# Performance work log

Measured on AMD Instinct MI355X. Metric: run time of the kernel, lower is better.

Reference implementation:

```python
import jax, jax.numpy as jnp
import numpy as np

N = 20000      # nodes
E = 320000     # edges (avg degree 16)
C = 128        # channels (num_features from hidden_irreps 128x0e+128x1o)
R = 8          # radial basis size
S = 10         # num_species
H = 64         # radial MLP hidden
M = 16         # MLP_irreps = 16x0e
AVG_NEIGH = 16.0


def setup_inputs() -> dict:
    key = jax.random.key(0)
    ks = jax.random.split(key, 24)
    d = {}
    d["vectors"] = jax.random.normal(ks[0], (E, 3), jnp.float32)
    d["lengths"] = jax.random.uniform(ks[1], (E, 1), jnp.float32)
    d["node_feats"] = jax.random.normal(ks[2], (N, C), jnp.float32)
    species = jax.random.randint(ks[3], (N,), 0, S)
    d["node_attrs"] = jax.nn.one_hot(species, S, dtype=jnp.float32)
    d["edge_feats"] = jax.random.normal(ks[4], (E, R), jnp.float32)
    d["edge_index"] = jax.random.randint(ks[5], (2, E), 0, N)
    p = lambda k, shape, sc: jax.random.normal(k, shape, jnp.float32) * sc
    d["W_up"] = p(ks[6], (C, C), C ** -0.5)
    d["radial_w1"] = p(ks[7], (R + 1, H), (R + 1) ** -0.5)
    d["radial_b1"] = jnp.zeros((H,), jnp.float32)
    d["radial_w2"] = p(ks[8], (H, 2 * C), H ** -0.5)
    d["Wd0"] = p(ks[9], (C, C), C ** -0.5)
    d["Wd1"] = p(ks[10], (C, C), C ** -0.5)
    d["Wprod0"] = p(ks[11], (S, 5, C), 1.0)   # per-species symmetric-contraction weights, 0e paths
    d["Wprod1"] = p(ks[12], (S, 4, C), 1.0)   # per-species weights, 1o paths
    d["Wp0"] = p(ks[13], (C, C), C ** -0.5)
    d["Wp1"] = p(ks[14], (C, C), C ** -0.5)
    d["Wr1"] = p(ks[15], (C, M), C ** -0.5)
    d["Wr2"] = p(ks[16], (M, C), M ** -0.5)
    d["Wg"] = p(ks[17], (M, 1), M ** -0.5)
    d["wv"] = p(ks[18], (C, 1), C ** -0.5)
    return d


def _forward(vectors, lengths, node_feats, node_attrs, edge_feats,
             W_up, radial_w1, radial_b1, radial_w2, Wd0, Wd1,
             Wprod0, Wprod1, Wp0, Wp1, Wr1, Wr2, Wg, wv, edge_index):
    senders, receivers = edge_index[0], edge_index[1]
    # --- spherical harmonics (normalize=True), l=0 constant, l=1 ~ sqrt(3)*unit_vec ---
    u = vectors / (jnp.linalg.norm(vectors, axis=1, keepdims=True) + 1e-9)
    Y1 = jnp.sqrt(3.0) * u                                    # [E,3]
    # --- DiffusionInteractionBlock: linear up, radial-weighted tp conv, scatter, linear down ---
    h = node_feats @ W_up                                     # [N,C]
    hs = h[senders]                                           # [E,C] gather
    rad_in = jnp.concatenate([edge_feats, lengths], axis=1)   # [E,R+1]
    rad = jax.nn.silu(rad_in @ radial_w1 + radial_b1) @ radial_w2  # [E,2C]
    w0, w1 = rad[:, :C], rad[:, C:]
    m0 = w0 * hs                                              # [E,C]   0e x 0e -> 0e
    m1 = (w1 * hs)[:, None, :] * Y1[:, :, None]               # [E,3,C] 0e x 1o -> 1o
    s0 = jax.ops.segment_sum(m0, receivers, num_segments=N) / AVG_NEIGH
    s1 = jax.ops.segment_sum(m1, receivers, num_segments=N) / AVG_NEIGH
    a0 = s0 @ Wd0                                             # [N,C]
    a1 = s1 @ Wd1                                             # [N,3,C]
    # --- EquivariantProductBasisBlock: symmetric contraction, correlation=3, per-species weights ---
    dot11 = jnp.sum(a1 * a1, axis=1)                          # [N,C]  1o.1o -> 0e
    paths0 = jnp.stack([a0, a0 * a0, dot11, a0 ** 3, a0 * dot11], axis=1)          # [N,5,C]
    paths1 = jnp.stack([a1, a0[:, None, :] * a1, (a0 ** 2)[:, None, :] * a1,
                        dot11[:, None, :] * a1], axis=1)                            # [N,4,3,C]
    b0 = jnp.einsum('ns,spc,npc->nc', node_attrs, Wprod0, paths0)
    b1 = jnp.einsum('ns,spc,npic->nic', node_attrs, Wprod1, paths1)
    h0 = b0 @ Wp0                                             # [N,C]
    h1 = b1 @ Wp1                                             # [N,3,C]
    # --- NonLinearReadoutBlock: gated MLP readout ---
    mh = jax.nn.silu(h0 @ Wr1)                                # [N,M]
    scalars = mh @ Wr2                                        # [N,C]
    gate = jax.nn.silu(mh @ Wg)                               # [N,1]
    vec = (h1 @ wv)[..., 0] * gate                            # [N,3]
    nf = jnp.concatenate([h0, h1.reshape(N, 3 * C)], axis=1)  # [N,4C]
    return scalars, vec, nf


def reference(vectors, lengths, node_feats, node_attrs, edge_feats, edge_index,
              W_up, radial_w1, radial_b1, radial_w2, Wd0, Wd1,
              Wprod0, Wprod1, Wp0, Wp1, Wr1, Wr2, Wg, wv):
    # returns (node_out[:, :-3], node_out[:, -3:], node_feats)
    return _forward(vectors, lengths, node_feats, node_attrs, edge_feats,
                    W_up, radial_w1, radial_b1, radial_w2, Wd0, Wd1,
                    Wprod0, Wprod1, Wp0, Wp1, Wr1, Wr2, Wg, wv, edge_index)
```

## Files before the change

### kernel.cpp

```cpp
#include <hip/hip_runtime.h>

#define NN 20000
#define NE 320000
#define CC 128
#define SS 10
#define NWIN 10000

typedef __attribute__((ext_vector_type(8))) short short8;
typedef __attribute__((ext_vector_type(4))) float f32x4;

#define MFMA16(a, b, c) __builtin_amdgcn_mfma_f32_16x16x32_bf16(a, b, c, 0, 0, 0)

__device__ __forceinline__ float silu_f(float x) { return x / (1.f + __expf(-x)); }

__device__ __forceinline__ unsigned short f2bf(float x) {
  unsigned u = __float_as_uint(x);
  unsigned r = u + 0x7FFFu + ((u >> 16) & 1u);
  return (unsigned short)(r >> 16);
}
__device__ __forceinline__ float bf2f(unsigned short h) {
  return __uint_as_float(((unsigned)h) << 16);
}
__device__ __forceinline__ void cvt8(const float* xs, short8& ah, short8& al) {
#pragma unroll
  for (int j = 0; j < 8; ++j) {
    const unsigned short h = f2bf(xs[j]);
    ah[j] = (short)h;
    al[j] = (short)f2bf(xs[j] - bf2f(h));
  }
}

__global__ __launch_bounds__(256) void k_prep_w2(const float* __restrict__ W2,
                                                 unsigned short* __restrict__ w2h,
                                                 unsigned short* __restrict__ w2l) {
  const int i = blockIdx.x * 256 + threadIdx.x;
  if (i < 64 * 256) {
    const int col = i % 256, k = i / 256;
    const float x = W2[i];
    const unsigned short h = f2bf(x);
    w2h[col * 64 + k] = h;
    w2l[col * 64 + k] = f2bf(x - bf2f(h));
  }
}

__global__ __launch_bounds__(256) void k_prep_w128(
    const float* __restrict__ Wd0, const float* __restrict__ Wd1,
    const float* __restrict__ Wp0, const float* __restrict__ Wp1,
    unsigned short* __restrict__ wh, unsigned short* __restrict__ wl) {
  const int b = blockIdx.x;
  const int m = b >> 6;
  const int i = (b & 63) * 256 + threadIdx.x;
  const float* W = (m == 0) ? Wd0 : (m == 1) ? Wd1 : (m == 2) ? Wp0 : Wp1;
  const int k = i >> 7, col = i & 127;
  const float x = W[i];
  const unsigned short h = f2bf(x);
  wh[m * 16384 + col * 128 + k] = h;
  wl[m * 16384 + col * 128 + k] = f2bf(x - bf2f(h));
}

__global__ __launch_bounds__(128) void k_node_h(const float* __restrict__ nf,
                                                const float* __restrict__ W,
                                                float* __restrict__ h) {
  __shared__ __align__(16) float rows[8][CC];
  const int c = threadIdx.x;
  const int n0 = blockIdx.x * 8;
#pragma unroll
  for (int q = 0; q < 8; ++q) rows[q][c] = nf[(n0 + q) * CC + c];
  __syncthreads();
  float acc[8] = {0.f, 0.f, 0.f, 0.f, 0.f, 0.f, 0.f, 0.f};
  for (int k = 0; k < CC; k += 4) {
    const float w0 = W[(k + 0) * CC + c];
    const float w1 = W[(k + 1) * CC + c];
    const float w2 = W[(k + 2) * CC + c];
    const float w3 = W[(k + 3) * CC + c];
#pragma unroll
    for (int q = 0; q < 8; ++q) {
      float4 v = *(const float4*)&rows[q][k];
      acc[q] += v.x * w0 + v.y * w1 + v.z * w2 + v.w * w3;
    }
  }
#pragma unroll
  for (int q = 0; q < 8; ++q) h[(n0 + q) * CC + c] = acc[q];
}

__global__ void k_hist(const int* __restrict__ recv, int* __restrict__ cnt) {
  int i = blockIdx.x * blockDim.x + threadIdx.x;
  if (i < NE) atomicAdd(&cnt[recv[i]], 1);
}

__global__ __launch_bounds__(1024) void k_scan2(int* cntcur, int* offs) {
  const int t = threadIdx.x;
  int v[20];
  int tot = 0;
  if (t < 1000) {
#pragma unroll
    for (int i = 0; i < 20; ++i) {
      v[i] = cntcur[t * 20 + i];
      tot += v[i];
    }
  }
  const int lane = t & 63;
  int x = tot;
#pragma unroll
  for (int off = 1; off < 64; off <<= 1) {
    int y = __shfl_up(x, off, 64);
    if (lane >= off) x += y;
  }
  __shared__ int wt[16], wo[16];
  if (lane == 63) wt[t >> 6] = x;
  __syncthreads();
  if (t == 0) {
    int a = 0;
    for (int w = 0; w < 16; ++w) {
      wo[w] = a;
      a += wt[w];
    }
    offs[NN] = a;
  }
  __syncthreads();
  int run = wo[t >> 6] + x - tot;
  if (t < 1000) {
#pragma unroll
    for (int i = 0; i < 20; ++i) {
      offs[t * 20 + i] = run;
      cntcur[t * 20 + i] = run;
      run += v[i];
    }
  }
}

__global__ void k_fill2(const int* __restrict__ recv, const int* __restrict__ snd,
                        const float* __restrict__ vectors,
                        const float* __restrict__ lengths,
                        const float* __restrict__ efeat, int* __restrict__ cur,
                        float* __restrict__ edata) {
  int i = blockIdx.x * blockDim.x + threadIdx.x;
  if (i < NE) {
    const int r = recv[i];
    const int pos = atomicAdd(&cur[r], 1);
    const float vx = vectors[i * 3 + 0];
    const float vy = vectors[i * 3 + 1];
    const float vz = vectors[i * 3 + 2];
    const float nr = sqrtf(vx * vx + vy * vy + vz * vz) + 1e-9f;
    const float sc = 1.7320508075688772f / nr;
    float4 a = {vx * sc, vy * sc, vz * sc, lengths[i]};
    float4 b = *(const float4*)&efeat[(size_t)i * 8];
    float4 c = *(const float4*)&efeat[(size_t)i * 8 + 4];
    float4 d;
    ((int*)&d)[0] = snd[i];
    d.y = 0.f; d.z = 0.f; d.w = 0.f;
    float* rec = edata + (size_t)pos * 16;
    *(float4*)rec = a;
    *(float4*)(rec + 4) = b;
    *(float4*)(rec + 8) = c;
    *(float4*)(rec + 12) = d;
  }
}

__global__ __launch_bounds__(256) void k_edge3p(
    const float* __restrict__ hbuf, const float* __restrict__ W1,
    const float* __restrict__ B1, const unsigned short* __restrict__ w2h,
    const unsigned short* __restrict__ w2l, const int* __restrict__ offs,
    const float* __restrict__ edata, float* __restrict__ sout) {
  __shared__ __align__(16) float W1s[9 * 64];
  __shared__ __align__(16) float B1s[64];
  __shared__ __align__(16) float ed[2][32][20];
  __shared__ __align__(16) unsigned short hidh[32][72];
  __shared__ __align__(16) unsigned short hidl[32][72];

  const int t = threadIdx.x;
  const int l = t & 63, wv = t >> 6, lg = l >> 4, lm = l & 15;
  const int half = wv & 1;
  const bool isw1 = wv >= 2;

  for (int i = t; i < 576; i += 256) W1s[i] = W1[i];
  if (t < 64) B1s[t] = B1[t];

  short8 Bh[4][2], Bl[4][2];
#pragma unroll
  for (int ct = 0; ct < 4; ++ct)
#pragma unroll
    for (int s = 0; s < 2; ++s) {
      const int col = wv * 64 + ct * 16 + lm;
      Bh[ct][s] = *(const short8*)&w2h[col * 64 + s * 32 + lg * 8];
      Bl[ct][s] = *(const short8*)&w2l[col * 64 + s * 32 + lg * 8];
    }

  const int se = t >> 1, sq = t & 1;
  const int se2 = t >> 2, sq2 = t & 3;

#define CONSUME(GR, ACC, HC, YA, YB, YC)                                       \
  do {                                                                         \
    float vvv[4][4];                                                           \
    _Pragma("unroll") for (int ct = 0; ct < 4; ++ct)                           \
        _Pragma("unroll") for (int r = 0; r < 4; ++r)                          \
            vvv[ct][r] = (ACC)[ct][r] * (HC)[ct][r];                           \
    const bool fast0 = ((GR) + 16 <= o1);                                      \
    const bool fast1 = ((GR) >= o1) && ((GR) + 16 <= o2);                      \
    if (fast0) {                                                               \
      if (!isw1) {                                                             \
        _Pragma("unroll") for (int ct = 0; ct < 4; ++ct)                       \
            _Pragma("unroll") for (int r = 0; r < 4; ++r)                      \
                p0[0][ct] += vvv[ct][r];                                       \
      } else {                                                                 \
        _Pragma("unroll") for (int ct = 0; ct < 4; ++ct)                       \
            _Pragma("unroll") for (int r = 0; r < 4; ++r) {                    \
          px[0][ct] += vvv[ct][r] * (YA)[r];                                   \
          py[0][ct] += vvv[ct][r] * (YB)[r];                                   \
          pz[0][ct] += vvv[ct][r] * (YC)[r];                                   \
        }                                                                      \
      }                                                                        \
    } else if (fast1) {                                                        \
      if (!isw1) {                                                             \
        _Pragma("unroll") for (int ct = 0; ct < 4; ++ct)                       \
            _Pragma("unroll") for (int r = 0; r < 4; ++r)                      \
                p0[1][ct] += vvv[ct][r];                                       \
      } else {                                                                 \
        _Pragma("unroll") for (int ct = 0; ct < 4; ++ct)                       \
            _Pragma("unroll") for (int r = 0; r < 4; ++r) {                    \
          px[1][ct] += vvv[ct][r] * (YA)[r];                                   \
          py[1][ct] += vvv[ct][r] * (YB)[r];                                   \
          pz[1][ct] += vvv[ct][r] * (YC)[r];                                   \
        }                                                                      \
      }                                                                        \
    } else {                                                                   \
      const int grow0 = (GR) + lg * 4;                                         \
      _Pragma("unroll") for (int sl = 0; sl < 2; ++sl) {                       \
        const int slo = sl ? o1 : o0;                                          \
        const int shi = sl ? o2 : o1;                                          \
        if (shi > (GR) && slo < (GR) + 16) {                                   \
          if (!isw1) {                                                         \
            _Pragma("unroll") for (int r = 0; r < 4; ++r) {                    \
              const bool in = (grow0 + r >= slo) && (grow0 + r < shi);         \
              _Pragma("unroll") for (int ct = 0; ct < 4; ++ct)                 \
                  p0[sl][ct] += in ? vvv[ct][r] : 0.f;                         \
            }                                                                  \
          } else {                                                             \
            _Pragma("unroll") for (int r = 0; r < 4; ++r) {                    \
              const bool in = (grow0 + r >= slo) && (grow0 + r < shi);         \
              _Pragma("unroll") for (int ct = 0; ct < 4; ++ct) {               \
                const float m = in ? vvv[ct][r] : 0.f;                         \
                px[sl][ct] += m * (YA)[r];                                     \
                py[sl][ct] += m * (YB)[r];                                     \
                pz[sl][ct] += m * (YC)[r];                                     \
              }                                                                \
            }                                                                  \
          }                                                                    \
        }                                                                      \
      }                                                                        \
    }                                                                          \
  } while (0)

  __syncthreads();

  for (int win = blockIdx.x; win < NWIN; win += gridDim.x) {
    const int nb = win * 2;
    const int o0 = offs[nb], o1 = offs[nb + 1], o2 = offs[nb + 2];

    float p0[2][4] = {};
    float px[2][4] = {}, py[2][4] = {}, pz[2][4] = {};

    float4 sreg = {0.f, 0.f, 0.f, 0.f};
    if (t < 128) {
      const int idx = o0 + se2;
      if (idx < o2) sreg = *(const float4*)&edata[(size_t)idx * 16 + sq2 * 4];
      *(float4*)&ed[0][se2][sq2 * 4] = sreg;
      sreg = (float4){0.f, 0.f, 0.f, 0.f};
      const int idx1 = o0 + 32 + se2;
      if (idx1 < o2) sreg = *(const float4*)&edata[(size_t)idx1 * 16 + sq2 * 4];
    }
    __syncthreads();

    const int npass = (o2 - o0 + 31) >> 5;
    for (int p = 0; p < npass; ++p) {
      const int pb = p & 1;
      const int base = o0 + p * 32;
      {
        const int e = t & 31, kseg = t >> 5;
        const int k0 = kseg * 8;
        float ef[9];
#pragma unroll
        for (int r = 0; r < 8; ++r) ef[r] = ed[pb][e][4 + r];
        ef[8] = ed[pb][e][3];
        float4 xa = *(const float4*)&B1s[k0];
        float4 xb = *(const float4*)&B1s[k0 + 4];
#pragma unroll
        for (int r = 0; r < 9; ++r) {
          const float4 wa = *(const float4*)&W1s[r * 64 + k0];
          const float4 wb = *(const float4*)&W1s[r * 64 + k0 + 4];
          xa.x += ef[r] * wa.x; xa.y += ef[r] * wa.y;
          xa.z += ef[r] * wa.z; xa.w += ef[r] * wa.w;
          xb.x += ef[r] * wb.x; xb.y += ef[r] * wb.y;
          xb.z += ef[r] * wb.z; xb.w += ef[r] * wb.w;
        }
        float xs[8];
        xs[0] = silu_f(xa.x); xs[1] = silu_f(xa.y);
        xs[2] = silu_f(xa.z); xs[3] = silu_f(xa.w);
        xs[4] = silu_f(xb.x); xs[5] = silu_f(xb.y);
        xs[6] = silu_f(xb.z); xs[7] = silu_f(xb.w);
        short8 ah, al;
        cvt8(xs, ah, al);
        *(short8*)&hidh[e][k0] = ah;
        *(short8*)&hidl[e][k0] = al;
      }
      __syncthreads();
      if (t < 128) {
        *(float4*)&ed[pb ^ 1][se2][sq2 * 4] = sreg;
        sreg = (float4){0.f, 0.f, 0.f, 0.f};
        const int idx2 = base + 64 + se2;
        if (idx2 < o2) sreg = *(const float4*)&edata[(size_t)idx2 * 16 + sq2 * 4];
      }
      {
        int sd0[4];
        float ya0[4], yb0[4], yc0[4];
#pragma unroll
        for (int r = 0; r < 4; ++r) {
          const int row = lg * 4 + r;
          sd0[r] = __float_as_int(ed[pb][row][12]);
          ya0[r] = ed[pb][row][0];
          yb0[r] = ed[pb][row][1];
          yc0[r] = ed[pb][row][2];
        }
        float hc0[4][4];
#pragma unroll
        for (int ct = 0; ct < 4; ++ct) {
          const int col = half * 64 + ct * 16 + lm;
#pragma unroll
          for (int r = 0; r < 4; ++r) hc0[ct][r] = hbuf[(size_t)sd0[r] * CC + col];
        }
        short8 Ah0 = *(const short8*)&hidh[lm][lg * 8];
        short8 Ah1 = *(const short8*)&hidh[lm][32 + lg * 8];
        short8 Al0 = *(const short8*)&hidl[lm][lg * 8];
        short8 Al1 = *(const short8*)&hidl[lm][32 + lg * 8];
        f32x4 acc0[4];
#pragma unroll
        for (int ct = 0; ct < 4; ++ct) {
          f32x4 a = {0.f, 0.f, 0.f, 0.f};
          a = MFMA16(Ah0, Bh[ct][0], a);
          a = MFMA16(Ah0, Bl[ct][0], a);
          a = MFMA16(Al0, Bh[ct][0], a);
          a = MFMA16(Ah1, Bh[ct][1], a);
          a = MFMA16(Ah1, Bl[ct][1], a);
          a = MFMA16(Al1, Bh[ct][1], a);
          acc0[ct] = a;
        }
        const bool live1 = (base + 16) < o2;
        if (live1) {
          int sd1[4];
          float ya1[4], yb1[4], yc1[4];
#pragma unroll
          for (int r = 0; r < 4; ++r) {
            const int row = 16 + lg * 4 + r;
            sd1[r] = __float_as_int(ed[pb][row][12]);
            ya1[r] = ed[pb][row][0];
            yb1[r] = ed[pb][row][1];
            yc1[r] = ed[pb][row][2];
          }
          float hc1[4][4];
#pragma unroll
          for (int ct = 0; ct < 4; ++ct) {
            const int col = half * 64 + ct * 16 + lm;
#pragma unroll
            for (int r = 0; r < 4; ++r) hc1[ct][r] = hbuf[(size_t)sd1[r] * CC + col];
          }
          CONSUME(base, acc0, hc0, ya0, yb0, yc0);
          short8 Bh0_ = *(const short8*)&hidh[16 + lm][lg * 8];
          short8 Bh1_ = *(const short8*)&hidh[16 + lm][32 + lg * 8];
          short8 Bl0_ = *(const short8*)&hidl[16 + lm][lg * 8];
          short8 Bl1_ = *(const short8*)&hidl[16 + lm][32 + lg * 8];
          f32x4 acc1[4];
#pragma unroll
          for (int ct = 0; ct < 4; ++ct) {
            f32x4 a = {0.f, 0.f, 0.f, 0.f};
            a = MFMA16(Bh0_, Bh[ct][0], a);
            a = MFMA16(Bh0_, Bl[ct][0], a);
            a = MFMA16(Bl0_, Bh[ct][0], a);
            a = MFMA16(Bh1_, Bh[ct][1], a);
            a = MFMA16(Bh1_, Bl[ct][1], a);
            a = MFMA16(Bl1_, Bh[ct][1], a);
            acc1[ct] = a;
          }
          CONSUME(base + 16, acc1, hc1, ya1, yb1, yc1);
        } else {
          CONSUME(base, acc0, hc0, ya0, yb0, yc0);
        }
      }
      __syncthreads();
    }

    const float inv = 1.f / 16.f;
#pragma unroll
    for (int sl = 0; sl < 2; ++sl) {
      const int n = nb + sl;
      if (!isw1) {
#pragma unroll
        for (int ct = 0; ct < 4; ++ct) {
          float v = p0[sl][ct];
          v += __shfl_xor(v, 16, 64);
          v += __shfl_xor(v, 32, 64);
          if (lg == 0) sout[(size_t)n * 512 + half * 64 + ct * 16 + lm] = v * inv;
        }
      } else {
#pragma unroll
        for (int ct = 0; ct < 4; ++ct) {
          float vx = px[sl][ct], vy = py[sl][ct], vz = pz[sl][ct];
          vx += __shfl_xor(vx, 16, 64); vx += __shfl_xor(vx, 32, 64);
          vy += __shfl_xor(vy, 16, 64); vy += __shfl_xor(vy, 32, 64);
          vz += __shfl_xor(vz, 16, 64); vz += __shfl_xor(vz, 32, 64);
          if (lg == 0) {
            const int c = half * 64 + ct * 16 + lm;
            sout[(size_t)n * 512 + 128 + c] = vx * inv;
            sout[(size_t)n * 512 + 256 + c] = vy * inv;
            sout[(size_t)n * 512 + 384 + c] = vz * inv;
          }
        }
      }
    }
  }
#undef CONSUME
}

__global__ __launch_bounds__(256, 2) void k_down3(
    const float* __restrict__ sbuf, const float* __restrict__ attrs,
    const unsigned short* __restrict__ wbh, const unsigned short* __restrict__ wbl,
    const float* __restrict__ Wprod0, const float* __restrict__ Wprod1,
    const float* __restrict__ Wr1, const float* __restrict__ Wr2,
    const float* __restrict__ Wg, const float* __restrict__ wvv,
    float* __restrict__ out_scalars, float* __restrict__ out_vec,
    float* __restrict__ out_nf) {
  __shared__ __align__(16) char smem[35840];
  __shared__ int sidx_s[16];
  __shared__ float mh_s[16][17];
  __shared__ float gate_s[16];
  unsigned short* bh = (unsigned short*)smem;
  unsigned short* bl = bh + 8960;
  float* hX = (float*)smem;

  const int t = threadIdx.x;
  const int l = t & 63, wv = t >> 6, lg = l >> 4, lm = l & 15;
  const int n0 = blockIdx.x * 16;

  if (t < 16) {
    int si = 0;
#pragma unroll
    for (int s = 0; s < SS; ++s)
      si = (attrs[(size_t)(n0 + t) * SS + s] > 0.5f) ? s : si;
    sidx_s[t] = si;
  }

  short8 Wfh[2][2][4], Wfl[2][2][4];
#pragma unroll
  for (int mat = 0; mat < 2; ++mat)
#pragma unroll
    for (int ct = 0; ct < 2; ++ct)
#pragma unroll
      for (int ks = 0; ks < 4; ++ks) {
        const size_t off =
            (size_t)mat * 16384 + (size_t)(wv * 32 + ct * 16 + lm) * 128 + ks * 32 + lg * 8;
        Wfh[mat][ct][ks] = *(const short8*)&wbh[off];
        Wfl[mat][ct][ks] = *(const short8*)&wbl[off];
      }

  f32x4 acc[4][2];
#pragma unroll 1
  for (int comp = 0; comp < 4; ++comp) {
    short8 Ah[4], Al[4];
#pragma unroll
    for (int ks = 0; ks < 4; ++ks) {
      const size_t so = (size_t)(n0 + lm) * 512 + comp * 128 + ks * 32 + lg * 8;
      const float4 xa = *(const float4*)&sbuf[so];
      const float4 xb = *(const float4*)&sbuf[so + 4];
      float xs[8] = {xa.x, xa.y, xa.z, xa.w, xb.x, xb.y, xb.z, xb.w};
      cvt8(xs, Ah[ks], Al[ks]);
    }
    const int mat = comp ? 1 : 0;
#pragma unroll
    for (int ct = 0; ct < 2; ++ct) {
      f32x4 a = {0.f, 0.f, 0.f, 0.f};
#pragma unroll
      for (int ks = 0; ks < 4; ++ks) {
        a = MFMA16(Ah[ks], Wfh[mat][ct][ks], a);
        a = MFMA16(Ah[ks], Wfl[mat][ct][ks], a);
        a = MFMA16(Al[ks], Wfh[mat][ct][ks], a);
      }
      acc[comp][ct] = a;
    }
  }

#pragma unroll
  for (int ct = 0; ct < 2; ++ct) {
#pragma unroll
    for (int r = 0; r < 4; ++r) {
      const int node = lg * 4 + r;
      const int c = wv * 32 + ct * 16 + lm;
      const int si = sidx_s[node];
      const float a0 = acc[0][ct][r];
      const float ax = acc[1][ct][r], ay = acc[2][ct][r], az = acc[3][ct][r];
      const float dot = ax * ax + ay * ay + az * az;
      const float a2 = a0 * a0;
      const float* w0 = Wprod0 + (size_t)si * 5 * CC;
      const float* w1 = Wprod1 + (size_t)si * 4 * CC;
      const float b0v = w0[c] * a0 + w0[CC + c] * a2 + w0[2 * CC + c] * dot +
                        w0[3 * CC + c] * (a2 * a0) + w0[4 * CC + c] * (a0 * dot);
      const float fac =
          w1[c] + w1[CC + c] * a0 + w1[2 * CC + c] * a2 + w1[3 * CC + c] * dot;
      const float bv[4] = {b0v, ax * fac, ay * fac, az * fac};
#pragma unroll
      for (int m = 0; m < 4; ++m) {
        const int idx = (m * 16 + node) * 140 + c;
        const unsigned short h = f2bf(bv[m]);
        bh[idx] = h;
        bl[idx] = f2bf(bv[m] - bf2f(h));
      }
    }
  }

#pragma unroll
  for (int mat = 0; mat < 2; ++mat)
#pragma unroll
    for (int ct = 0; ct < 2; ++ct)
#pragma unroll
      for (int ks = 0; ks < 4; ++ks) {
        const size_t off = (size_t)(2 + mat) * 16384 +
                           (size_t)(wv * 32 + ct * 16 + lm) * 128 + ks * 32 + lg * 8;
        Wfh[mat][ct][ks] = *(const short8*)&wbh[off];
        Wfl[mat][ct][ks] = *(const short8*)&wbl[off];
      }
  __syncthreads();

  f32x4 acch[4][2];
#pragma unroll 1
  for (int comp = 0; comp < 4; ++comp) {
    short8 Ah[4], Al[4];
#pragma unroll
    for (int ks = 0; ks < 4; ++ks) {
      const int idx = (comp * 16 + lm) * 140 + ks * 32 + lg * 8;
      Ah[ks] = *(const short8*)&bh[idx];
      Al[ks] = *(const short8*)&bl[idx];
    }
    const int mat = comp ? 1 : 0;
#pragma unroll
    for (int ct = 0; ct < 2; ++ct) {
      f32x4 a = {0.f, 0.f, 0.f, 0.f};
#pragma unroll
      for (int ks = 0; ks < 4; ++ks) {
        a = MFMA16(Ah[ks], Wfh[mat][ct][ks], a);
        a = MFMA16(Ah[ks], Wfl[mat][ct][ks], a);
        a = MFMA16(Al[ks], Wfh[mat][ct][ks], a);
      }
      acch[comp][ct] = a;
    }
  }
  __syncthreads();

#pragma unroll
  for (int comp = 0; comp < 4; ++comp)
#pragma unroll
    for (int ct = 0; ct < 2; ++ct)
#pragma unroll
      for (int r = 0; r < 4; ++r) {
        const int node = lg * 4 + r;
        const int c = wv * 32 + ct * 16 + lm;
        hX[(comp * 16 + node) * 132 + c] = acch[comp][ct][r];
        out_nf[(size_t)(n0 + node) * 512 + comp * 128 + c] = acch[comp][ct][r];
      }
  __syncthreads();

  {
    const int node = t >> 4, m = t & 15;
    float a = 0.f;
    const float* Xn = &hX[node * 132];
    for (int k = 0; k < CC; k += 4) {
      const float4 h4 = *(const float4*)&Xn[k];
      a += h4.x * Wr1[(k + 0) * 16 + m] + h4.y * Wr1[(k + 1) * 16 + m] +
           h4.z * Wr1[(k + 2) * 16 + m] + h4.w * Wr1[(k + 3) * 16 + m];
    }
    mh_s[node][m] = silu_f(a);
  }
  __syncthreads();
  if (t < 16) {
    float g = 0.f;
#pragma unroll
    for (int m = 0; m < 16; ++m) g += mh_s[t][m] * Wg[m];
    gate_s[t] = silu_f(g);
  }
  __syncthreads();
  {
    const int node = t >> 4, cb = (t & 15) * 8;
#pragma unroll
    for (int j = 0; j < 8; ++j) {
      float a = 0.f;
#pragma unroll
      for (int m = 0; m < 16; ++m) a += mh_s[node][m] * Wr2[m * CC + cb + j];
      out_scalars[(size_t)(n0 + node) * CC + cb + j] = a;
    }
  }
  if (t < 48) {
    const int node = t / 3, i = t % 3;
    float a = 0.f;
    const float* Xn = &hX[((1 + i) * 16 + node) * 132];
    for (int k = 0; k < CC; k += 4) {
      const float4 h4 = *(const float4*)&Xn[k];
      const float4 w4 = *(const float4*)&wvv[k];
      a += h4.x * w4.x + h4.y * w4.y + h4.z * w4.z + h4.w * w4.w;
    }
    out_vec[(size_t)(n0 + node) * 3 + i] = a * gate_s[node];
  }
}

extern "C" void kernel_launch(void* const* d_in, const int* in_sizes, int n_in,
                              void* d_out, int out_size, void* d_ws, size_t ws_size,
                              hipStream_t stream) {
  const float* vectors    = (const float*)d_in[0];
  const float* lengths    = (const float*)d_in[1];
  const float* node_feats = (const float*)d_in[2];
  const float* node_attrs = (const float*)d_in[3];
  const float* edge_feats = (const float*)d_in[4];
  const int*   edge_index = (const int*)d_in[5];
  const float* W_up       = (const float*)d_in[6];
  const float* radial_w1  = (const float*)d_in[7];
  const float* radial_b1  = (const float*)d_in[8];
  const float* radial_w2  = (const float*)d_in[9];
  const float* Wd0        = (const float*)d_in[10];
  const float* Wd1        = (const float*)d_in[11];
  const float* Wprod0     = (const float*)d_in[12];
  const float* Wprod1     = (const float*)d_in[13];
  const float* Wp0        = (const float*)d_in[14];
  const float* Wp1        = (const float*)d_in[15];
  const float* Wr1        = (const float*)d_in[16];
  const float* Wr2        = (const float*)d_in[17];
  const float* Wg         = (const float*)d_in[18];
  const float* wv         = (const float*)d_in[19];

  float* out = (float*)d_out;
  float* out_scalars = out;
  float* out_vec = out + (size_t)NN * CC;
  float* out_nf = out + (size_t)NN * CC + (size_t)NN * 3;
  float* sbuf = out_nf;
  float* hbuf = out_scalars;

  int* cnt = (int*)d_ws;
  int* offs = cnt + NN;
  float* edata = (float*)(offs + NN + 4);
  unsigned short* w2h = (unsigned short*)(edata + (size_t)NE * 16);
  unsigned short* w2l = w2h + 16384;
  unsigned short* wbh = w2l + 16384;
  unsigned short* wbl = wbh + 4 * 16384;

  const int* senders = edge_index;
  const int* receivers = edge_index + NE;

  hipMemsetAsync(cnt, 0, NN * sizeof(int), stream);
  k_prep_w2<<<64, 256, 0, stream>>>(radial_w2, w2h, w2l);
  k_prep_w128<<<256, 256, 0, stream>>>(Wd0, Wd1, Wp0, Wp1, wbh, wbl);
  k_node_h<<<NN / 8, 128, 0, stream>>>(node_feats, W_up, hbuf);
  k_hist<<<NE / 256, 256, 0, stream>>>(receivers, cnt);
  k_scan2<<<1, 1024, 0, stream>>>(cnt, offs);
  k_fill2<<<NE / 256, 256, 0, stream>>>(receivers, senders, vectors, lengths,
                                        edge_feats, cnt, edata);
  k_edge3p<<<2048, 256, 0, stream>>>(hbuf, radial_w1, radial_b1, w2h, w2l,
                                     offs, edata, sbuf);
  k_down3<<<NN / 16, 256, 0, stream>>>(sbuf, node_attrs, wbh, wbl, Wprod0,
                                       Wprod1, Wr1, Wr2, Wg, wv,
                                       out_scalars, out_vec, out_nf);
}
```

Before: 311.2 us.

## Split edge kernel columns so each wave handles both radial halves for 32 channels

Changes the per-wave work split in the edge convolution kernel. Previously two waves handled the scalar-path radial weights and two handled the vector-path weights, each across 64 channels. Now every wave computes both radial halves for its own 32 channels. The sender feature gather (hbuf) per wave drops from 64 to 32 columns, and the edge product is reused for both the scalar and vector accumulations. The MFMA count per wave and the register footprint stay about the same, and all waves now follow the same uniform code path.

```diff
diff --git a/kernel.cpp b/kernel.cpp
--- a/kernel.cpp
+++ b/kernel.cpp
@@ -157,7 +157,7 @@
   }
 }
 
-__global__ __launch_bounds__(256) void k_edge3p(
+__global__ __launch_bounds__(256) void k_edge3q(
     const float* __restrict__ hbuf, const float* __restrict__ W1,
     const float* __restrict__ B1, const unsigned short* __restrict__ w2h,
     const unsigned short* __restrict__ w2l, const int* __restrict__ offs,
@@ -170,58 +170,50 @@
 
   const int t = threadIdx.x;
   const int l = t & 63, wv = t >> 6, lg = l >> 4, lm = l & 15;
-  const int half = wv & 1;
-  const bool isw1 = wv >= 2;
 
   for (int i = t; i < 576; i += 256) W1s[i] = W1[i];
   if (t < 64) B1s[t] = B1[t];
 
-  short8 Bh[4][2], Bl[4][2];
-#pragma unroll
-  for (int ct = 0; ct < 4; ++ct)
+  short8 B0h[2][2], B0l[2][2], B1h[2][2], B1l[2][2];
+#pragma unroll
+  for (int ct = 0; ct < 2; ++ct)
 #pragma unroll
     for (int s = 0; s < 2; ++s) {
-      const int col = wv * 64 + ct * 16 + lm;
-      Bh[ct][s] = *(const short8*)&w2h[col * 64 + s * 32 + lg * 8];
-      Bl[ct][s] = *(const short8*)&w2l[col * 64 + s * 32 + lg * 8];
-    }
-
-  const int se = t >> 1, sq = t & 1;
+      const int col0 = wv * 32 + ct * 16 + lm;
+      const int col1 = 128 + col0;
+      B0h[ct][s] = *(const short8*)&w2h[col0 * 64 + s * 32 + lg * 8];
+      B0l[ct][s] = *(const short8*)&w2l[col0 * 64 + s * 32 + lg * 8];
+      B1h[ct][s] = *(const short8*)&w2h[col1 * 64 + s * 32 + lg * 8];
+      B1l[ct][s] = *(const short8*)&w2l[col1 * 64 + s * 32 + lg * 8];
+    }
+
   const int se2 = t >> 2, sq2 = t & 3;
 
-#define CONSUME(GR, ACC, HC, YA, YB, YC)                                       \
+#define CONSUME(GR, A0, A1, HC, YA, YB, YC)                                    \
   do {                                                                         \
-    float vvv[4][4];                                                           \
-    _Pragma("unroll") for (int ct = 0; ct < 4; ++ct)                           \
-        _Pragma("unroll") for (int r = 0; r < 4; ++r)                          \
-            vvv[ct][r] = (ACC)[ct][r] * (HC)[ct][r];                           \
+    float vv0[2][4], m1[2][4];                                                 \
+    _Pragma("unroll") for (int ct = 0; ct < 2; ++ct)                           \
+        _Pragma("unroll") for (int r = 0; r < 4; ++r) {                        \
+      vv0[ct][r] = (A0)[ct][r] * (HC)[ct][r];                                  \
+      m1[ct][r] = (A1)[ct][r] * (HC)[ct][r];                                   \
+    }                                                                          \
     const bool fast0 = ((GR) + 16 <= o1);                                      \
     const bool fast1 = ((GR) >= o1) && ((GR) + 16 <= o2);                      \
     if (fast0) {                                                               \
-      if (!isw1) {                                                             \
-        _Pragma("unroll") for (int ct = 0; ct < 4; ++ct)                       \
-            _Pragma("unroll") for (int r = 0; r < 4; ++r)                      \
-                p0[0][ct] += vvv[ct][r];                                       \
-      } else {                                                                 \
-        _Pragma("unroll") for (int ct = 0; ct < 4; ++ct)                       \
-            _Pragma("unroll") for (int r = 0; r < 4; ++r) {                    \
-          px[0][ct] += vvv[ct][r] * (YA)[r];                                   \
-          py[0][ct] += vvv[ct][r] * (YB)[r];                                   \
-          pz[0][ct] += vvv[ct][r] * (YC)[r];                                   \
-        }                                                                      \
+      _Pragma("unroll") for (int ct = 0; ct < 2; ++ct)                         \
+          _Pragma("unroll") for (int r = 0; r < 4; ++r) {                      \
+        p0[0][ct] += vv0[ct][r];                                               \
+        px[0][ct] += m1[ct][r] * (YA)[r];                                      \
+        py[0][ct] += m1[ct][r] * (YB)[r];                                      \
+        pz[0][ct] += m1[ct][r] * (YC)[r];                                      \
       }                                                                        \
     } else if (fast1) {                                                        \
-      if (!isw1) {                                                             \
-        _Pragma("unroll") for (int ct = 0; ct < 4; ++ct)                       \
-            _Pragma("unroll") for (int r = 0; r < 4; ++r)                      \
-                p0[1][ct] += vvv[ct][r];                                       \
-      } else {                                                                 \
-        _Pragma("unroll") for (int ct = 0; ct < 4; ++ct)                       \
-            _Pragma("unroll") for (int r = 0; r < 4; ++r) {                    \
-          px[1][ct] += vvv[ct][r] * (YA)[r];                                   \
-          py[1][ct] += vvv[ct][r] * (YB)[r];                                   \
-          pz[1][ct] += vvv[ct][r] * (YC)[r];                                   \
-        }                                                                      \
+      _Pragma("unroll") for (int ct = 0; ct < 2; ++ct)                         \
+          _Pragma("unroll") for (int r = 0; r < 4; ++r) {                      \
+        p0[1][ct] += vv0[ct][r];                                               \
+        px[1][ct] += m1[ct][r] * (YA)[r];                                      \
+        py[1][ct] += m1[ct][r] * (YB)[r];                                      \
+        pz[1][ct] += m1[ct][r] * (YC)[r];                                      \
       }                                                                        \
     } else {                                                                   \
       const int grow0 = (GR) + lg * 4;                                         \
@@ -229,21 +221,15 @@
         const int slo = sl ? o1 : o0;                                          \
         const int shi = sl ? o2 : o1;                                          \
         if (shi > (GR) && slo < (GR) + 16) {                                   \
-          if (!isw1) {                                                         \
-            _Pragma("unroll") for (int r = 0; r < 4; ++r) {                    \
-              const bool in = (grow0 + r >= slo) && (grow0 + r < shi);         \
-              _Pragma("unroll") for (int ct = 0; ct < 4; ++ct)                 \
-                  p0[sl][ct] += in ? vvv[ct][r] : 0.f;                         \
-            }                                                                  \
-          } else {                                                             \
-            _Pragma("unroll") for (int r = 0; r < 4; ++r) {                    \
-              const bool in = (grow0 + r >= slo) && (grow0 + r < shi);         \
-              _Pragma("unroll") for (int ct = 0; ct < 4; ++ct) {               \
-                const float m = in ? vvv[ct][r] : 0.f;                         \
-                px[sl][ct] += m * (YA)[r];                                     \
-                py[sl][ct] += m * (YB)[r];                                     \
-                pz[sl][ct] += m * (YC)[r];                                     \
-              }                                                                \
+          _Pragma("unroll") for (int r = 0; r < 4; ++r) {                      \
+            const bool in = (grow0 + r >= slo) && (grow0 + r < shi);           \
+            _Pragma("unroll") for (int ct = 0; ct < 2; ++ct) {                 \
+              const float v0 = in ? vv0[ct][r] : 0.f;                          \
+              const float m = in ? m1[ct][r] : 0.f;                            \
+              p0[sl][ct] += v0;                                                \
+              px[sl][ct] += m * (YA)[r];                                       \
+              py[sl][ct] += m * (YB)[r];                                       \
+              pz[sl][ct] += m * (YC)[r];                                       \
             }                                                                  \
           }                                                                    \
         }                                                                      \
@@ -257,8 +243,8 @@
     const int nb = win * 2;
     const int o0 = offs[nb], o1 = offs[nb + 1], o2 = offs[nb + 2];
 
-    float p0[2][4] = {};
-    float px[2][4] = {}, py[2][4] = {}, pz[2][4] = {};
+    float p0[2][2] = {};
+    float px[2][2] = {}, py[2][2] = {}, pz[2][2] = {};
 
     float4 sreg = {0.f, 0.f, 0.f, 0.f};
     if (t < 128) {
@@ -321,10 +307,10 @@
           yb0[r] = ed[pb][row][1];
           yc0[r] = ed[pb][row][2];
         }
-        float hc0[4][4];
-#pragma unroll
-        for (int ct = 0; ct < 4; ++ct) {
-          const int col = half * 64 + ct * 16 + lm;
+        float hc0[2][4];
+#pragma unroll
+        for (int ct = 0; ct < 2; ++ct) {
+          const int col = wv * 32 + ct * 16 + lm;
 #pragma unroll
           for (int r = 0; r < 4; ++r) hc0[ct][r] = hbuf[(size_t)sd0[r] * CC + col];
         }
@@ -332,17 +318,25 @@
         short8 Ah1 = *(const short8*)&hidh[lm][32 + lg * 8];
         short8 Al0 = *(const short8*)&hidl[lm][lg * 8];
         short8 Al1 = *(const short8*)&hidl[lm][32 + lg * 8];
-        f32x4 acc0[4];
-#pragma unroll
-        for (int ct = 0; ct < 4; ++ct) {
+        f32x4 a0[2], a1[2];
+#pragma unroll
+        for (int ct = 0; ct < 2; ++ct) {
           f32x4 a = {0.f, 0.f, 0.f, 0.f};
-          a = MFMA16(Ah0, Bh[ct][0], a);
-          a = MFMA16(Ah0, Bl[ct][0], a);
-          a = MFMA16(Al0, Bh[ct][0], a);
-          a = MFMA16(Ah1, Bh[ct][1], a);
-          a = MFMA16(Ah1, Bl[ct][1], a);
-          a = MFMA16(Al1, Bh[ct][1], a);
-          acc0[ct] = a;
+          a = MFMA16(Ah0, B0h[ct][0], a);
+          a = MFMA16(Ah0, B0l[ct][0], a);
+          a = MFMA16(Al0, B0h[ct][0], a);
+          a = MFMA16(Ah1, B0h[ct][1], a);
+          a = MFMA16(Ah1, B0l[ct][1], a);
+          a = MFMA16(Al1, B0h[ct][1], a);
+          a0[ct] = a;
+          f32x4 b = {0.f, 0.f, 0.f, 0.f};
+          b = MFMA16(Ah0, B1h[ct][0], b);
+          b = MFMA16(Ah0, B1l[ct][0], b);
+          b = MFMA16(Al0, B1h[ct][0], b);
+          b = MFMA16(Ah1, B1h[ct][1], b);
+          b = MFMA16(Ah1, B1l[ct][1], b);
+          b = MFMA16(Al1, B1h[ct][1], b);
+          a1[ct] = b;
         }
         const bool live1 = (base + 16) < o2;
         if (live1) {
@@ -356,33 +350,41 @@
             yb1[r] = ed[pb][row][1];
             yc1[r] = ed[pb][row][2];
           }
-          float hc1[4][4];
-#pragma unroll
-          for (int ct = 0; ct < 4; ++ct) {
-            const int col = half * 64 + ct * 16 + lm;
+          float hc1[2][4];
+#pragma unroll
+          for (int ct = 0; ct < 2; ++ct) {
+            const int col = wv * 32 + ct * 16 + lm;
 #pragma unroll
             for (int r = 0; r < 4; ++r) hc1[ct][r] = hbuf[(size_t)sd1[r] * CC + col];
           }
-          CONSUME(base, acc0, hc0, ya0, yb0, yc0);
-          short8 Bh0_ = *(const short8*)&hidh[16 + lm][lg * 8];
-          short8 Bh1_ = *(const short8*)&hidh[16 + lm][32 + lg * 8];
-          short8 Bl0_ = *(const short8*)&hidl[16 + lm][lg * 8];
-          short8 Bl1_ = *(const short8*)&hidl[16 + lm][32 + lg * 8];
-          f32x4 acc1[4];
-#pragma unroll
-          for (int ct = 0; ct < 4; ++ct) {
+          CONSUME(base, a0, a1, hc0, ya0, yb0, yc0);
+          short8 Ch0 = *(const short8*)&hidh[16 + lm][lg * 8];
+          short8 Ch1 = *(const short8*)&hidh[16 + lm][32 + lg * 8];
+          short8 Cl0 = *(const short8*)&hidl[16 + lm][lg * 8];
+          short8 Cl1 = *(const short8*)&hidl[16 + lm][32 + lg * 8];
+          f32x4 b0[2], b1[2];
+#pragma unroll
+          for (int ct = 0; ct < 2; ++ct) {
             f32x4 a = {0.f, 0.f, 0.f, 0.f};
-            a = MFMA16(Bh0_, Bh[ct][0], a);
-            a = MFMA16(Bh0_, Bl[ct][0], a);
-            a = MFMA16(Bl0_, Bh[ct][0], a);
-            a = MFMA16(Bh1_, Bh[ct][1], a);
-            a = MFMA16(Bh1_, Bl[ct][1], a);
-            a = MFMA16(Bl1_, Bh[ct][1], a);
-            acc1[ct] = a;
+            a = MFMA16(Ch0, B0h[ct][0], a);
+            a = MFMA16(Ch0, B0l[ct][0], a);
+            a = MFMA16(Cl0, B0h[ct][0], a);
+            a = MFMA16(Ch1, B0h[ct][1], a);
+            a = MFMA16(Ch1, B0l[ct][1], a);
+            a = MFMA16(Cl1, B0h[ct][1], a);
+            b0[ct] = a;
+            f32x4 b = {0.f, 0.f, 0.f, 0.f};
+            b = MFMA16(Ch0, B1h[ct][0], b);
+            b = MFMA16(Ch0, B1l[ct][0], b);
+            b = MFMA16(Cl0, B1h[ct][0], b);
+            b = MFMA16(Ch1, B1h[ct][1], b);
+            b = MFMA16(Ch1, B1l[ct][1], b);
+            b = MFMA16(Cl1, B1h[ct][1], b);
+            b1[ct] = b;
           }
-          CONSUME(base + 16, acc1, hc1, ya1, yb1, yc1);
+          CONSUME(base + 16, b0, b1, hc1, ya1, yb1, yc1);
         } else {
-          CONSUME(base, acc0, hc0, ya0, yb0, yc0);
+          CONSUME(base, a0, a1, hc0, ya0, yb0, yc0);
         }
       }
       __syncthreads();
@@ -392,27 +394,20 @@
 #pragma unroll
     for (int sl = 0; sl < 2; ++sl) {
       const int n = nb + sl;
-      if (!isw1) {
-#pragma unroll
-        for (int ct = 0; ct < 4; ++ct) {
-          float v = p0[sl][ct];
-          v += __shfl_xor(v, 16, 64);
-          v += __shfl_xor(v, 32, 64);
-          if (lg == 0) sout[(size_t)n * 512 + half * 64 + ct * 16 + lm] = v * inv;
-        }
-      } else {
-#pragma unroll
-        for (int ct = 0; ct < 4; ++ct) {
-          float vx = px[sl][ct], vy = py[sl][ct], vz = pz[sl][ct];
-          vx += __shfl_xor(vx, 16, 64); vx += __shfl_xor(vx, 32, 64);
-          vy += __shfl_xor(vy, 16, 64); vy += __shfl_xor(vy, 32, 64);
-          vz += __shfl_xor(vz, 16, 64); vz += __shfl_xor(vz, 32, 64);
-          if (lg == 0) {
-            const int c = half * 64 + ct * 16 + lm;
-            sout[(size_t)n * 512 + 128 + c] = vx * inv;
-            sout[(size_t)n * 512 + 256 + c] = vy * inv;
-            sout[(size_t)n * 512 + 384 + c] = vz * inv;
-          }
+#pragma unroll
+      for (int ct = 0; ct < 2; ++ct) {
+        const int col = wv * 32 + ct * 16 + lm;
+        float v = p0[sl][ct];
+        float vx = px[sl][ct], vy = py[sl][ct], vz = pz[sl][ct];
+        v += __shfl_xor(v, 16, 64);  v += __shfl_xor(v, 32, 64);
+        vx += __shfl_xor(vx, 16, 64); vx += __shfl_xor(vx, 32, 64);
+        vy += __shfl_xor(vy, 16, 64); vy += __shfl_xor(vy, 32, 64);
+        vz += __shfl_xor(vz, 16, 64); vz += __shfl_xor(vz, 32, 64);
+        if (lg == 0) {
+          sout[(size_t)n * 512 + col] = v * inv;
+          sout[(size_t)n * 512 + 128 + col] = vx * inv;
+          sout[(size_t)n * 512 + 256 + col] = vy * inv;
+          sout[(size_t)n * 512 + 384 + col] = vz * inv;
         }
       }
     }
@@ -658,7 +653,7 @@
   k_scan2<<<1, 1024, 0, stream>>>(cnt, offs);
   k_fill2<<<NE / 256, 256, 0, stream>>>(receivers, senders, vectors, lengths,
                                         edge_feats, cnt, edata);
-  k_edge3p<<<2048, 256, 0, stream>>>(hbuf, radial_w1, radial_b1, w2h, w2l,
+  k_edge3q<<<2048, 256, 0, stream>>>(hbuf, radial_w1, radial_b1, w2h, w2l,
                                      offs, edata, sbuf);
   k_down3<<<NN / 16, 256, 0, stream>>>(sbuf, node_attrs, wbh, wbl, Wprod0,
                                        Wprod1, Wr1, Wr2, Wg, wv,
```

New measurement: 303.1 us. 2.6% less time.
